# Optimization experiments

Measured on AMD Instinct MI355X. Metric: run time of the kernel, lower is better.

Reference implementation:

```python
import jax, jax.numpy as jnp
import numpy as np

B, H, WD = 4, 1440, 1440      # batch, BEV grid (sparse_shape)
N, C, NB = 200000, 32, 3      # active voxels, channels, num basic blocks
EPS = 1e-3                    # BatchNorm1d eps in the module


def setup_inputs() -> dict:
    key = jax.random.key(0)
    ks = jax.random.split(key, 10)
    feats = jax.random.normal(ks[0], (N, C), jnp.float32)
    coords_b = jax.random.randint(ks[1], (N,), 0, B, dtype=jnp.int32)
    coords_y = jax.random.randint(ks[2], (N,), 0, H, dtype=jnp.int32)
    coords_x = jax.random.randint(ks[3], (N,), 0, WD, dtype=jnp.int32)
    # [block, conv(2), tap(3x3=9), Cin, Cout]; fan-in scaled init
    Wk = jax.random.normal(ks[4], (NB, 2, 9, C, C), jnp.float32) / np.sqrt(9 * C)
    bias = 0.01 * jax.random.normal(ks[5], (NB, 2, C), jnp.float32)
    gamma = 1.0 + 0.1 * jax.random.normal(ks[6], (NB, 2, C), jnp.float32)
    beta = 0.1 * jax.random.normal(ks[7], (NB, 2, C), jnp.float32)
    mean = 0.1 * jax.random.normal(ks[8], (NB, 2, C), jnp.float32)
    var = jax.random.uniform(ks[9], (NB, 2, C), jnp.float32, 0.5, 1.5)
    return dict(feats=feats, Wk=Wk, bias=bias, gamma=gamma, beta=beta,
                mean=mean, var=var, coords_b=coords_b, coords_y=coords_y,
                coords_x=coords_x)


def _build_rulebook(coords_b, coords_y, coords_x):
    # Dense hash: grid cell -> voxel row id (-1 if empty). Shared by all
    # submanifold convs in the stage (same indice_key in the original).
    idx_map = jnp.full((B, H, WD), -1, jnp.int32)
    idx_map = idx_map.at[coords_b, coords_y, coords_x].set(
        jnp.arange(N, dtype=jnp.int32))
    offs = jnp.array([(dy, dx) for dy in (-1, 0, 1) for dx in (-1, 0, 1)],
                     jnp.int32)                      # [9,2]
    ny = coords_y[None, :] + offs[:, 0:1]            # [9,N]
    nx = coords_x[None, :] + offs[:, 1:2]
    inb = (ny >= 0) & (ny < H) & (nx >= 0) & (nx < WD)
    nyc = jnp.clip(ny, 0, H - 1)
    nxc = jnp.clip(nx, 0, WD - 1)
    nidx = idx_map[jnp.broadcast_to(coords_b[None, :], (9, N)), nyc, nxc]
    mask = inb & (nidx >= 0)
    nidx = jnp.where(mask, nidx, 0)                  # safe gather index
    return nidx, mask[..., None].astype(jnp.float32)


def reference(feats, Wk, bias, gamma, beta, mean, var,
              coords_b, coords_y, coords_x):
    nidx, maskf = _build_rulebook(coords_b, coords_y, coords_x)

    def subm(x, w, b):
        # gather-GEMM-scatter submanifold 3x3 conv on active sites only
        g = x[nidx] * maskf                          # [9,N,Cin]
        return jnp.einsum('knc,kco->no', g, w) + b   # [N,Cout]

    def bn(x, g_, b_, m_, v_):
        return (x - m_) * jax.lax.rsqrt(v_ + EPS) * g_ + b_

    h = feats
    for i in range(NB):  # SparseBasicBlock stack (fixed small layer count)
        identity = h
        o = jax.nn.relu(bn(subm(h, Wk[i, 0], bias[i, 0]),
                           gamma[i, 0], beta[i, 0], mean[i, 0], var[i, 0]))
        o = bn(subm(o, Wk[i, 1], bias[i, 1]),
               gamma[i, 1], beta[i, 1], mean[i, 1], var[i, 1])
        h = jax.nn.relu(o + identity)
    return h
```

## Files before the change

kernel.cpp:

```cpp
#include <hip/hip_runtime.h>

#define NB_ 3
#define CB 4
#define CH 1440
#define CW 1440
#define NC 32
#define EPSV 1e-3f

typedef __attribute__((ext_vector_type(8))) short bf16x8;
typedef __attribute__((ext_vector_type(16))) float f32x16;

union U16 { uint4 u; bf16x8 v; };

__device__ __forceinline__ unsigned pk2(float a, float b) {
    unsigned ua = __float_as_uint(a), ub = __float_as_uint(b);
    ua += 0x7fffu + ((ua >> 16) & 1u);
    ub += 0x7fffu + ((ub >> 16) & 1u);
    return (ua >> 16) | (ub & 0xffff0000u);
}
__device__ __forceinline__ float bfl(unsigned u) { return __uint_as_float(u << 16); }
__device__ __forceinline__ float bfh(unsigned u) { return __uint_as_float(u & 0xffff0000u); }

__global__ __launch_bounds__(256) void k_clear(
    const int* __restrict__ cb, const int* __restrict__ cy, const int* __restrict__ cx,
    int* __restrict__ idx_map, unsigned* __restrict__ pkey, int n)
{
    int i = blockIdx.x * blockDim.x + threadIdx.x;
    if (i >= n) return;
    unsigned key = ((unsigned)cb[i] * CH + (unsigned)cy[i]) * CW + (unsigned)cx[i];
    pkey[i] = key;
    idx_map[key] = -1;
}

__global__ __launch_bounds__(256) void k_build_map(
    const unsigned* __restrict__ pkey, int* __restrict__ idx_map, int n)
{
    int i = blockIdx.x * blockDim.x + threadIdx.x;
    if (i < n) atomicMax(&idx_map[pkey[i]], i);
}

__device__ __forceinline__ int vquery(const int* __restrict__ idx_map,
                                      const unsigned* __restrict__ pkey,
                                      unsigned cell, int n)
{
    int v = idx_map[cell];
    if (v < 0 || v >= n) return -1;
    return (pkey[v] == cell) ? v : -1;
}

__global__ __launch_bounds__(256) void k_prep(
    const unsigned* __restrict__ pkey, const int* __restrict__ idx_map,
    int* __restrict__ roff,
    const float* __restrict__ feats, unsigned short* __restrict__ xbf,
    const float* __restrict__ Wk, uint4* __restrict__ Bfg,
    const float* __restrict__ bias, const float* __restrict__ gamma,
    const float* __restrict__ beta, const float* __restrict__ mean,
    const float* __restrict__ var, float* __restrict__ sh_all,
    unsigned short* __restrict__ z0, unsigned short* __restrict__ z1,
    unsigned short* __restrict__ z2, int n)
{
    int RB = (n + 255) >> 8;
    int CVT = ((n * NC / 8) + 255) >> 8;
    int bx = blockIdx.x;

    if (bx < RB) {
        int i = bx * 256 + threadIdx.x;
        if (i >= n) return;
        unsigned key = pkey[i];
        unsigned x = key % CW;
        unsigned y = (key / CW) % CH;
        roff[4 * n + i] = idx_map[key] * 64;
        #pragma unroll
        for (int k = 0; k < 9; ++k) {
            if (k == 4) continue;
            int dy = k / 3 - 1, dx = k % 3 - 1;
            int ny = (int)y + dy, nx = (int)x + dx;
            int nb = -1;
            if (ny >= 0 && ny < CH && nx >= 0 && nx < CW)
                nb = vquery(idx_map, pkey, key + dy * CW + dx, n);
            roff[k * n + i] = (nb >= 0) ? nb * 64 : -1;
        }
    } else if (bx < RB + CVT) {
        int i = ((bx - RB) * 256 + threadIdx.x) * 8;
        if (i + 8 <= n * NC) {
            float4 a0 = *(const float4*)(feats + i);
            float4 a1 = *(const float4*)(feats + i + 4);
            uint4 r;
            r.x = pk2(a0.x, a0.y); r.y = pk2(a0.z, a0.w);
            r.z = pk2(a1.x, a1.y); r.w = pk2(a1.z, a1.w);
            *(uint4*)(xbf + i) = r;
        }
    } else {
        int wb = bx - RB - CVT;
        if (wb == 0 && threadIdx.x < 12) {
            uint4 z = make_uint4(0, 0, 0, 0);
            int tt = threadIdx.x;
            if (tt < 4)       ((uint4*)z0)[tt] = z;
            else if (tt < 8)  ((uint4*)z1)[tt - 4] = z;
            else              ((uint4*)z2)[tt - 8] = z;
        }
        int t = wb * 256 + threadIdx.x;
        if (t >= 6 * 9 * 2 * 64) return;
        int l = t & 63, h = (t >> 6) & 1;
        int rest = t >> 7;
        int k = rest % 9, layer = rest / 9;
        int o = l & 31;
        int lo = layer * 32 + o;
        float scv = gamma[lo] * rsqrtf(var[lo] + EPSV);
        if (k == 0 && h == 0 && l < 32)
            sh_all[lo] = (bias[lo] - mean[lo]) * scv + beta[lo];
        int c0 = h * 16 + 8 * (l >> 5);
        const float* wp = Wk + (size_t)layer * 9216 + k * 1024 + o;
        uint4 r;
        r.x = pk2(wp[(c0 + 0) * 32] * scv, wp[(c0 + 1) * 32] * scv);
        r.y = pk2(wp[(c0 + 2) * 32] * scv, wp[(c0 + 3) * 32] * scv);
        r.z = pk2(wp[(c0 + 4) * 32] * scv, wp[(c0 + 5) * 32] * scv);
        r.w = pk2(wp[(c0 + 6) * 32] * scv, wp[(c0 + 7) * 32] * scv);
        Bfg[t] = r;
    }
}

template<bool ADD_ID, bool F32OUT>
__global__ __launch_bounds__(256, 6) void k_conv(
    const unsigned short* __restrict__ in,
    const unsigned short* __restrict__ idn,
    void* __restrict__ outv,
    const uint4* __restrict__ Bf,
    const float* __restrict__ sh,
    const int* __restrict__ roff, int n)
{
    int l = threadIdx.x & 63, wv = threadIdx.x >> 6;
    int q = l & 31, h5 = l >> 5;

    int ntile = (n + 31) >> 5;
    int tile = blockIdx.x * 4 + wv;
    if (tile >= ntile) return;

    const int zoff = n * 64;
    const char* inB = (const char*)in;

    int p0 = tile << 5;
    int pr = p0 + q;
    bool rowok = pr < n;
    int prc = rowok ? pr : n - 1;

    int rk[9];
    #pragma unroll
    for (int k = 0; k < 9; ++k) rk[k] = roff[(size_t)k * n + prc];

    f32x16 acc = {0.f,0.f,0.f,0.f,0.f,0.f,0.f,0.f,0.f,0.f,0.f,0.f,0.f,0.f,0.f,0.f};

    #pragma unroll
    for (int g = 0; g < 3; ++g) {
        bool act[3];
        U16 a0[3], a1[3];
        #pragma unroll
        for (int j = 0; j < 3; ++j) {
            int k = g * 3 + j;
            act[j] = __any(rk[k] >= 0);
            if (act[j]) {
                int off = (rowok && rk[k] >= 0) ? rk[k] : zoff;
                const char* ap = inB + off + h5 * 16;
                a0[j].u = *(const uint4*)(ap);
                a1[j].u = *(const uint4*)(ap + 32);
            }
        }
        #pragma unroll
        for (int j = 0; j < 3; ++j) {
            int k = g * 3 + j;
            if (act[j]) {
                U16 b0, b1;
                b0.u = Bf[(k * 2 + 0) * 64 + l];
                b1.u = Bf[(k * 2 + 1) * 64 + l];
                acc = __builtin_amdgcn_mfma_f32_32x32x16_bf16(b0.v, a0[j].v, acc, 0, 0, 0);
                acc = __builtin_amdgcn_mfma_f32_32x32x16_bf16(b1.v, a1[j].v, acc, 0, 0, 0);
            }
        }
    }

    if (rowok) {
        #pragma unroll
        for (int g = 0; g < 4; ++g) {
            int ch = g * 8 + 4 * h5;
            float4 s4 = *(const float4*)(sh + ch);
            float y0 = acc[g * 4 + 0] + s4.x;
            float y1 = acc[g * 4 + 1] + s4.y;
            float y2 = acc[g * 4 + 2] + s4.z;
            float y3 = acc[g * 4 + 3] + s4.w;
            if (ADD_ID) {
                uint2 iv = *(const uint2*)(idn + (size_t)pr * 32 + ch);
                y0 += bfl(iv.x); y1 += bfh(iv.x);
                y2 += bfl(iv.y); y3 += bfh(iv.y);
            }
            y0 = fmaxf(y0, 0.f); y1 = fmaxf(y1, 0.f);
            y2 = fmaxf(y2, 0.f); y3 = fmaxf(y3, 0.f);
            if (F32OUT) {
                *(float4*)((float*)outv + (size_t)pr * 32 + ch) =
                    make_float4(y0, y1, y2, y3);
            } else {
                uint2 r;
                r.x = pk2(y0, y1); r.y = pk2(y2, y3);
                *(uint2*)((unsigned short*)outv + (size_t)pr * 32 + ch) = r;
            }
        }
    }
}

extern "C" void kernel_launch(void* const* d_in, const int* in_sizes, int n_in,
                              void* d_out, int out_size, void* d_ws, size_t ws_size,
                              hipStream_t stream)
{
    const float* feats = (const float*)d_in[0];
    const float* Wk    = (const float*)d_in[1];
    const float* bias  = (const float*)d_in[2];
    const float* gamma = (const float*)d_in[3];
    const float* beta  = (const float*)d_in[4];
    const float* mean  = (const float*)d_in[5];
    const float* var   = (const float*)d_in[6];
    const int* cb = (const int*)d_in[7];
    const int* cy = (const int*)d_in[8];
    const int* cx = (const int*)d_in[9];
    float* out = (float*)d_out;
    int n = in_sizes[0] / NC;

    char* ws = (char*)d_ws;
    int*            idx_map = (int*)(ws + 0);
    unsigned*       pkey    = (unsigned*)(ws + 33177600);
    int*            roff    = (int*)(ws + 33977600);
    uint4*          Bfg     = (uint4*)(ws + 41177600);
    float*          sh_all  = (float*)(ws + 41288192);
    unsigned short* xbf     = (unsigned short*)(ws + 41288960);
    unsigned short* tmpbf   = (unsigned short*)(ws + 54089024);
    unsigned short* hb      = (unsigned short*)(ws + 66889088);

    int RB  = (n + 255) / 256;
    int CVT = ((n * NC / 8) + 255) / 256;
    k_clear<<<RB, 256, 0, stream>>>(cb, cy, cx, idx_map, pkey, n);
    k_build_map<<<RB, 256, 0, stream>>>(pkey, idx_map, n);
    k_prep<<<RB + CVT + 27, 256, 0, stream>>>(
        pkey, idx_map, roff, feats, xbf, Wk, Bfg,
        bias, gamma, beta, mean, var, sh_all,
        xbf + (size_t)n * 32, tmpbf + (size_t)n * 32, hb + (size_t)n * 32, n);

    const int ntile = (n + 31) / 32;
    const int G = (ntile + 3) / 4;
    const int BSZ = 9 * 2 * 64;

    k_conv<false, false><<<G, 256, 0, stream>>>(xbf, nullptr, tmpbf,
        Bfg + 0 * BSZ, sh_all + 0,   roff, n);
    k_conv<true,  false><<<G, 256, 0, stream>>>(tmpbf, xbf, hb,
        Bfg + 1 * BSZ, sh_all + 32,  roff, n);
    k_conv<false, false><<<G, 256, 0, stream>>>(hb, nullptr, tmpbf,
        Bfg + 2 * BSZ, sh_all + 64,  roff, n);
    k_conv<true,  false><<<G, 256, 0, stream>>>(tmpbf, hb, xbf,
        Bfg + 3 * BSZ, sh_all + 96,  roff, n);
    k_conv<false, false><<<G, 256, 0, stream>>>(xbf, nullptr, tmpbf,
        Bfg + 4 * BSZ, sh_all + 128, roff, n);
    k_conv<true,  true><<<G, 256, 0, stream>>>(tmpbf, xbf, out,
        Bfg + 5 * BSZ, sh_all + 160, roff, n);
}
```

Baseline: 128.9 us.

## Reorder voxels by spatial row via counting sort to improve gather locality

Adds a histogram, a single-block scan and a rank pass that counting-sort the active voxels by (batch, y) row. Features are converted to bf16 in the sorted order, the rulebook offsets are remapped to sorted ranks, and the final conv scatters outputs back to the original row order. Neighbouring voxels then sit close together in memory, which is meant to make the 3x3 gathers in the six conv kernels hit cache more often. The cost is three extra small kernels plus a memset, and the sort order within a row is nondeterministic because ranks come from atomics.

```diff
diff --git a/kernel.cpp b/kernel.cpp
--- a/kernel.cpp
+++ b/kernel.cpp
@@ -1,11 +1,12 @@
 #include <hip/hip_runtime.h>
 
-#define NB_ 3
 #define CB 4
 #define CH 1440
 #define CW 1440
 #define NC 32
 #define EPSV 1e-3f
+#define NBKT (CB * CH)
+#define BSZ (9 * 2 * 64)
 
 typedef __attribute__((ext_vector_type(8))) short bf16x8;
 typedef __attribute__((ext_vector_type(16))) float f32x16;
@@ -21,22 +22,70 @@
 __device__ __forceinline__ float bfl(unsigned u) { return __uint_as_float(u << 16); }
 __device__ __forceinline__ float bfh(unsigned u) { return __uint_as_float(u & 0xffff0000u); }
 
-__global__ __launch_bounds__(256) void k_clear(
+__global__ __launch_bounds__(256) void k_hist(
     const int* __restrict__ cb, const int* __restrict__ cy, const int* __restrict__ cx,
-    int* __restrict__ idx_map, unsigned* __restrict__ pkey, int n)
+    int* __restrict__ idx_map, unsigned* __restrict__ pkey, int* __restrict__ hist,
+    int n)
 {
     int i = blockIdx.x * blockDim.x + threadIdx.x;
     if (i >= n) return;
     unsigned key = ((unsigned)cb[i] * CH + (unsigned)cy[i]) * CW + (unsigned)cx[i];
     pkey[i] = key;
     idx_map[key] = -1;
-}
-
-__global__ __launch_bounds__(256) void k_build_map(
-    const unsigned* __restrict__ pkey, int* __restrict__ idx_map, int n)
+    atomicAdd(&hist[key / CW], 1);
+}
+
+__global__ __launch_bounds__(1024) void k_scan(
+    const int* __restrict__ hist, int* __restrict__ bstart, int* __restrict__ bcnt,
+    unsigned short* __restrict__ z0, unsigned short* __restrict__ z1,
+    unsigned short* __restrict__ z2, int n)
+{
+    __shared__ int ps[1024];
+    int tid = threadIdx.x;
+    const int PB = 6;
+    int base = tid * PB;
+    int loc[PB]; int s = 0;
+    #pragma unroll
+    for (int j = 0; j < PB; ++j) {
+        int idx = base + j;
+        int v = (idx < NBKT) ? hist[idx] : 0;
+        loc[j] = s; s += v;
+    }
+    ps[tid] = s;
+    __syncthreads();
+    for (int off = 1; off < 1024; off <<= 1) {
+        int u = (tid >= off) ? ps[tid - off] : 0;
+        __syncthreads();
+        ps[tid] += u;
+        __syncthreads();
+    }
+    int excl = (tid > 0) ? ps[tid - 1] : 0;
+    #pragma unroll
+    for (int j = 0; j < PB; ++j)
+        if (base + j < NBKT) bstart[base + j] = excl + loc[j];
+    for (int i = tid; i < NBKT; i += 1024) bcnt[i] = 0;
+    if (tid < 12) {
+        uint4 z = make_uint4(0, 0, 0, 0);
+        if (tid < 4)       ((uint4*)(z0 + (size_t)n * 32))[tid] = z;
+        else if (tid < 8)  ((uint4*)(z1 + (size_t)n * 32))[tid - 4] = z;
+        else               ((uint4*)(z2 + (size_t)n * 32))[tid - 8] = z;
+    }
+}
+
+__global__ __launch_bounds__(256) void k_rank(
+    const unsigned* __restrict__ pkey, const int* __restrict__ bstart,
+    int* __restrict__ bcnt, int* __restrict__ rankof, int* __restrict__ sortidx,
+    unsigned* __restrict__ skey, int* __restrict__ idx_map, int n)
 {
     int i = blockIdx.x * blockDim.x + threadIdx.x;
-    if (i < n) atomicMax(&idx_map[pkey[i]], i);
+    if (i >= n) return;
+    unsigned key = pkey[i];
+    int bu = key / CW;
+    int r = bstart[bu] + atomicAdd(&bcnt[bu], 1);
+    rankof[i] = r;
+    sortidx[r] = i;
+    skey[r] = key;
+    atomicMax(&idx_map[key], i);
 }
 
 __device__ __forceinline__ int vquery(const int* __restrict__ idx_map,
@@ -49,27 +98,26 @@
 }
 
 __global__ __launch_bounds__(256) void k_prep(
-    const unsigned* __restrict__ pkey, const int* __restrict__ idx_map,
-    int* __restrict__ roff,
+    const unsigned* __restrict__ pkey, const unsigned* __restrict__ skey,
+    const int* __restrict__ idx_map, const int* __restrict__ rankof,
+    const int* __restrict__ sortidx, int* __restrict__ roff,
     const float* __restrict__ feats, unsigned short* __restrict__ xbf,
     const float* __restrict__ Wk, uint4* __restrict__ Bfg,
     const float* __restrict__ bias, const float* __restrict__ gamma,
     const float* __restrict__ beta, const float* __restrict__ mean,
-    const float* __restrict__ var, float* __restrict__ sh_all,
-    unsigned short* __restrict__ z0, unsigned short* __restrict__ z1,
-    unsigned short* __restrict__ z2, int n)
+    const float* __restrict__ var, float* __restrict__ sh_all, int n)
 {
     int RB = (n + 255) >> 8;
-    int CVT = ((n * NC / 8) + 255) >> 8;
+    int CVT = (n * 2 + 255) >> 8;
     int bx = blockIdx.x;
 
     if (bx < RB) {
-        int i = bx * 256 + threadIdx.x;
-        if (i >= n) return;
-        unsigned key = pkey[i];
+        int r = bx * 256 + threadIdx.x;
+        if (r >= n) return;
+        unsigned key = skey[r];
         unsigned x = key % CW;
         unsigned y = (key / CW) % CH;
-        roff[4 * n + i] = idx_map[key] * 64;
+        roff[4 * n + r] = rankof[idx_map[key]] * 64;
         #pragma unroll
         for (int k = 0; k < 9; ++k) {
             if (k == 4) continue;
@@ -78,28 +126,27 @@
             int nb = -1;
             if (ny >= 0 && ny < CH && nx >= 0 && nx < CW)
                 nb = vquery(idx_map, pkey, key + dy * CW + dx, n);
-            roff[k * n + i] = (nb >= 0) ? nb * 64 : -1;
+            roff[k * n + r] = (nb >= 0) ? rankof[nb] * 64 : -1;
         }
     } else if (bx < RB + CVT) {
-        int i = ((bx - RB) * 256 + threadIdx.x) * 8;
-        if (i + 8 <= n * NC) {
-            float4 a0 = *(const float4*)(feats + i);
-            float4 a1 = *(const float4*)(feats + i + 4);
-            uint4 r;
-            r.x = pk2(a0.x, a0.y); r.y = pk2(a0.z, a0.w);
-            r.z = pk2(a1.x, a1.y); r.w = pk2(a1.z, a1.w);
-            *(uint4*)(xbf + i) = r;
+        int t = (bx - RB) * 256 + threadIdx.x;
+        if (t < n * 2) {
+            int r = t >> 1, half = t & 1;
+            const float* src = feats + (size_t)sortidx[r] * 32 + half * 16;
+            float4 a0 = *(const float4*)(src);
+            float4 a1 = *(const float4*)(src + 4);
+            float4 a2 = *(const float4*)(src + 8);
+            float4 a3 = *(const float4*)(src + 12);
+            uint4 r0, r1;
+            r0.x = pk2(a0.x, a0.y); r0.y = pk2(a0.z, a0.w);
+            r0.z = pk2(a1.x, a1.y); r0.w = pk2(a1.z, a1.w);
+            r1.x = pk2(a2.x, a2.y); r1.y = pk2(a2.z, a2.w);
+            r1.z = pk2(a3.x, a3.y); r1.w = pk2(a3.z, a3.w);
+            *(uint4*)(xbf + (size_t)r * 32 + half * 16) = r0;
+            *(uint4*)(xbf + (size_t)r * 32 + half * 16 + 8) = r1;
         }
     } else {
-        int wb = bx - RB - CVT;
-        if (wb == 0 && threadIdx.x < 12) {
-            uint4 z = make_uint4(0, 0, 0, 0);
-            int tt = threadIdx.x;
-            if (tt < 4)       ((uint4*)z0)[tt] = z;
-            else if (tt < 8)  ((uint4*)z1)[tt - 4] = z;
-            else              ((uint4*)z2)[tt - 8] = z;
-        }
-        int t = wb * 256 + threadIdx.x;
+        int t = (bx - RB - CVT) * 256 + threadIdx.x;
         if (t >= 6 * 9 * 2 * 64) return;
         int l = t & 63, h = (t >> 6) & 1;
         int rest = t >> 7;
@@ -127,7 +174,7 @@
     void* __restrict__ outv,
     const uint4* __restrict__ Bf,
     const float* __restrict__ sh,
-    const int* __restrict__ roff, int n)
+    const int* __restrict__ roff, const int* __restrict__ sortidx, int n)
 {
     int l = threadIdx.x & 63, wv = threadIdx.x >> 6;
     int q = l & 31, h5 = l >> 5;
@@ -179,6 +226,7 @@
     }
 
     if (rowok) {
+        int orow = F32OUT ? sortidx[pr] : pr;
         #pragma unroll
         for (int g = 0; g < 4; ++g) {
             int ch = g * 8 + 4 * h5;
@@ -195,7 +243,7 @@
             y0 = fmaxf(y0, 0.f); y1 = fmaxf(y1, 0.f);
             y2 = fmaxf(y2, 0.f); y3 = fmaxf(y3, 0.f);
             if (F32OUT) {
-                *(float4*)((float*)outv + (size_t)pr * 32 + ch) =
+                *(float4*)((float*)outv + (size_t)orow * 32 + ch) =
                     make_float4(y0, y1, y2, y3);
             } else {
                 uint2 r;
@@ -229,33 +277,42 @@
     int*            roff    = (int*)(ws + 33977600);
     uint4*          Bfg     = (uint4*)(ws + 41177600);
     float*          sh_all  = (float*)(ws + 41288192);
-    unsigned short* xbf     = (unsigned short*)(ws + 41288960);
-    unsigned short* tmpbf   = (unsigned short*)(ws + 54089024);
-    unsigned short* hb      = (unsigned short*)(ws + 66889088);
+    int*            hist    = (int*)(ws + 41288960);
+    int*            bcnt    = (int*)(ws + 41312000);
+    int*            bstart  = (int*)(ws + 41335040);
+    int*            rankof  = (int*)(ws + 41358080);
+    int*            sortidx = (int*)(ws + 42158080);
+    unsigned*       skey    = (unsigned*)(ws + 42958080);
+    unsigned short* xbf     = (unsigned short*)(ws + 43758080);
+    unsigned short* tmpbf   = (unsigned short*)(ws + 56558144);
+    unsigned short* hb      = (unsigned short*)(ws + 69358208);
+
+    (void)hipMemsetAsync(hist, 0, 23040 * 2, stream);
 
     int RB  = (n + 255) / 256;
-    int CVT = ((n * NC / 8) + 255) / 256;
-    k_clear<<<RB, 256, 0, stream>>>(cb, cy, cx, idx_map, pkey, n);
-    k_build_map<<<RB, 256, 0, stream>>>(pkey, idx_map, n);
+    int CVT = (n * 2 + 255) / 256;
+    k_hist<<<RB, 256, 0, stream>>>(cb, cy, cx, idx_map, pkey, hist, n);
+    k_scan<<<1, 1024, 0, stream>>>(hist, bstart, bcnt,
+        xbf, tmpbf, hb, n);
+    k_rank<<<RB, 256, 0, stream>>>(pkey, bstart, bcnt, rankof, sortidx, skey,
+        idx_map, n);
     k_prep<<<RB + CVT + 27, 256, 0, stream>>>(
-        pkey, idx_map, roff, feats, xbf, Wk, Bfg,
-        bias, gamma, beta, mean, var, sh_all,
-        xbf + (size_t)n * 32, tmpbf + (size_t)n * 32, hb + (size_t)n * 32, n);
+        pkey, skey, idx_map, rankof, sortidx, roff, feats, xbf, Wk, Bfg,
+        bias, gamma, beta, mean, var, sh_all, n);
 
     const int ntile = (n + 31) / 32;
     const int G = (ntile + 3) / 4;
-    const int BSZ = 9 * 2 * 64;
 
     k_conv<false, false><<<G, 256, 0, stream>>>(xbf, nullptr, tmpbf,
-        Bfg + 0 * BSZ, sh_all + 0,   roff, n);
+        Bfg + 0 * BSZ, sh_all + 0,   roff, sortidx, n);
     k_conv<true,  false><<<G, 256, 0, stream>>>(tmpbf, xbf, hb,
-        Bfg + 1 * BSZ, sh_all + 32,  roff, n);
+        Bfg + 1 * BSZ, sh_all + 32,  roff, sortidx, n);
     k_conv<false, false><<<G, 256, 0, stream>>>(hb, nullptr, tmpbf,
-        Bfg + 2 * BSZ, sh_all + 64,  roff, n);
+        Bfg + 2 * BSZ, sh_all + 64,  roff, sortidx, n);
     k_conv<true,  false><<<G, 256, 0, stream>>>(tmpbf, hb, xbf,
-        Bfg + 3 * BSZ, sh_all + 96,  roff, n);
+        Bfg + 3 * BSZ, sh_all + 96,  roff, sortidx, n);
     k_conv<false, false><<<G, 256, 0, stream>>>(xbf, nullptr, tmpbf,
-        Bfg + 4 * BSZ, sh_all + 128, roff, n);
-    k_conv<true,  true><<<G, 256, 0, stream>>>(tmpbf, xbf, out,
-        Bfg + 5 * BSZ, sh_all + 160, roff, n);
-}
+        Bfg + 4 * BSZ, sh_all + 128, roff, sortidx, n);
+    k_conv<true,  true ><<<G, 256, 0, stream>>>(tmpbf, xbf, out,
+        Bfg + 5 * BSZ, sh_all + 160, roff, sortidx, n);
+}
```

Result: slower. 153.1 us (+18.8%).
